# Performance work log

Hardware: AMD Instinct MI355X
Metric: run time of the kernel (lower is better)

The kernel has to match this reference:

```python
import jax, jax.numpy as jnp
import numpy as np

N_NODES = 1_000_000
N_EDGES = 20_000_000


def setup_inputs() -> dict:
    key = jax.random.key(0)
    k_row, k_col, k_attr = jax.random.split(key, 3)
    # Guarantee every row appears at least once so row-sums are > 0
    # (the original module implicitly assumes no zero-degree rows).
    row_tail = jax.random.randint(k_row, (N_EDGES - N_NODES,), 0, N_NODES, dtype=jnp.int32)
    row = jnp.concatenate([jnp.arange(N_NODES, dtype=jnp.int32), row_tail])
    col = jax.random.randint(k_col, (N_EDGES,), 0, N_NODES, dtype=jnp.int32)
    edge_index = jnp.stack([row, col])  # [2, E]
    # Positive edge weights keep the reciprocal well-conditioned.
    edge_attr = jax.random.uniform(k_attr, (N_EDGES,), dtype=jnp.float32,
                                   minval=0.1, maxval=1.0)
    return {"edge_index": edge_index, "edge_attr": edge_attr, "N": N_NODES}


def reference(edge_index, edge_attr, N):
    # spmm(edge_index, edge_attr, N, N, ones) == per-row sum of edge weights
    rowsum = jax.ops.segment_sum(edge_attr, edge_index[0], num_segments=N)  # [N]
    rownorm = 1.0 / rowsum                                                  # [N]
    # Gather normalization factor at the COLUMN index of each edge, then scale.
    return rownorm[edge_index[1]] * edge_attr                                # [E]
```

## Files before the change

kernel.cpp:

```cpp
#include <hip/hip_runtime.h>
#include <hip/hip_fp16.h>
#include <stdint.h>


typedef int      v4i __attribute__((ext_vector_type(4)));
typedef float    v4f __attribute__((ext_vector_type(4)));
typedef unsigned v4u __attribute__((ext_vector_type(4)));
using ull = unsigned long long;
using u16 = unsigned short;

#define BKT_BITS 13
#define BKT_W    (1 << BKT_BITS)
#define NB       128
#define NMAX     (NB << BKT_BITS)
#define TILE     4096
#define BLOCK1   512
#define BLOCK2   512


__global__ __launch_bounds__(BLOCK1) void hist_kernel(
    const int* __restrict__ row, int* __restrict__ histG, int E)
{
    __shared__ int h[NB];
    const int t = threadIdx.x;
    const long base = (long)blockIdx.x * TILE;
    if (t < NB) h[t] = 0;
    __syncthreads();
    if (base + TILE <= (long)E) {
        #pragma unroll
        for (int k = 0; k < 2; ++k) {
            const long e0 = base + ((long)(k * BLOCK1 + t) << 2);
            const v4i rv = *reinterpret_cast<const v4i*>(row + e0);
            atomicAdd(&h[rv.x >> BKT_BITS], 1);
            atomicAdd(&h[rv.y >> BKT_BITS], 1);
            atomicAdd(&h[rv.z >> BKT_BITS], 1);
            atomicAdd(&h[rv.w >> BKT_BITS], 1);
        }
    } else {
        for (int k = 0; k < 2; ++k) {
            const long e0 = base + ((long)(k * BLOCK1 + t) << 2);
            for (int j = 0; j < 4; ++j)
                if (e0 + j < (long)E) atomicAdd(&h[row[e0 + j] >> BKT_BITS], 1);
        }
    }
    __syncthreads();
    if (t < NB) histG[(size_t)blockIdx.x * NB + t] = h[t];
}

__global__ __launch_bounds__(256) void totals_kernel(
    const int* __restrict__ histG, int* __restrict__ totals, int nTiles)
{
    __shared__ int s[256];
    const int b = blockIdx.x;
    int acc = 0;
    for (int t = threadIdx.x; t < nTiles; t += 256)
        acc += histG[(size_t)t * NB + b];
    s[threadIdx.x] = acc;
    __syncthreads();
    for (int o = 128; o > 0; o >>= 1) {
        if (threadIdx.x < o) s[threadIdx.x] += s[threadIdx.x + o];
        __syncthreads();
    }
    if (threadIdx.x == 0) totals[b] = s[0];
}

__global__ __launch_bounds__(NB) void bases_kernel(
    const int* __restrict__ totals, int* __restrict__ bases)
{
    __shared__ int s[NB];
    const int t = threadIdx.x;
    const int rc = (totals[t] + 1) & ~1;
    s[t] = rc;
    __syncthreads();
    for (int off = 1; off < NB; off <<= 1) {
        const int v = (t >= off) ? s[t - off] : 0;
        __syncthreads();
        s[t] += v;
        __syncthreads();
    }
    bases[t] = s[t] - rc;
}

__global__ __launch_bounds__(256) void offsets_kernel(
    const int* __restrict__ histG, const int* __restrict__ bases,
    int* __restrict__ offG, int nTiles)
{
    __shared__ int s[256];
    const int b = blockIdx.x;
    const int seg = (nTiles + 255) >> 8;
    const int t0 = threadIdx.x * seg;
    int acc = 0;
    for (int k = 0; k < seg; ++k) {
        const int t = t0 + k;
        if (t < nTiles) acc += histG[(size_t)t * NB + b];
    }
    s[threadIdx.x] = acc;
    __syncthreads();
    for (int off = 1; off < 256; off <<= 1) {
        const int v = (threadIdx.x >= off) ? s[threadIdx.x - off] : 0;
        __syncthreads();
        s[threadIdx.x] += v;
        __syncthreads();
    }
    int run = bases[b] + s[threadIdx.x] - acc;
    for (int k = 0; k < seg; ++k) {
        const int t = t0 + k;
        if (t < nTiles) {
            offG[(size_t)t * NB + b] = run;
            run += histG[(size_t)t * NB + b];
        }
    }
}

__global__ __launch_bounds__(BLOCK1) void scatter_kernel(
    const int* __restrict__ row, const float* __restrict__ attr,
    const int* __restrict__ offG, ull* __restrict__ pairsG, int E)
{
    __shared__ int cnt[NB];
    __shared__ int scanb[NB];
    __shared__ int gbase[NB];
    __shared__ ull pairs[TILE];

    const int  t    = threadIdx.x;
    const long base = (long)blockIdx.x * TILE;
    const bool full = (base + TILE <= (long)E);

    if (t < NB) cnt[t] = 0;
    __syncthreads();

    int r[8]; float a[8]; int rk[8];
    if (full) {
        #pragma unroll
        for (int k = 0; k < 2; ++k) {
            const long e0 = base + ((long)(k * BLOCK1 + t) << 2);
            const v4i rv = *reinterpret_cast<const v4i*>(row + e0);
            const v4f av = __builtin_nontemporal_load(reinterpret_cast<const v4f*>(attr + e0));
            r[k*4+0]=rv.x; r[k*4+1]=rv.y; r[k*4+2]=rv.z; r[k*4+3]=rv.w;
            a[k*4+0]=av.x; a[k*4+1]=av.y; a[k*4+2]=av.z; a[k*4+3]=av.w;
        }
        #pragma unroll
        for (int i = 0; i < 8; ++i)
            rk[i] = atomicAdd(&cnt[r[i] >> BKT_BITS], 1);
    } else {
        for (int k = 0; k < 2; ++k) {
            const long e0 = base + ((long)(k * BLOCK1 + t) << 2);
            for (int j = 0; j < 4; ++j) {
                const int i = k*4 + j;
                if (e0 + j < (long)E) {
                    r[i] = row[e0 + j]; a[i] = attr[e0 + j];
                    rk[i] = atomicAdd(&cnt[r[i] >> BKT_BITS], 1);
                } else r[i] = -1;
            }
        }
    }
    __syncthreads();

    if (t < 64) {
        const int h0 = cnt[2*t], h1 = cnt[2*t+1];
        const int sum = h0 + h1;
        int x = sum;
        #pragma unroll
        for (int off = 1; off < 64; off <<= 1) {
            const int y = __shfl_up(x, off);
            if (t >= off) x += y;
        }
        const int excl = x - sum;
        scanb[2*t]   = excl;
        scanb[2*t+1] = excl + h0;
    }
    if (t < NB) gbase[t] = offG[(size_t)blockIdx.x * NB + t];
    __syncthreads();

    #pragma unroll
    for (int i = 0; i < 8; ++i)
        if (r[i] >= 0)
            pairs[scanb[r[i] >> BKT_BITS] + rk[i]] =
                ((ull)__float_as_uint(a[i]) << 32) | (unsigned)r[i];
    __syncthreads();

    const int total = full ? TILE : (int)((long)E - base);
    for (int s = t; s < total; s += BLOCK1) {
        const ull p  = pairs[s];
        const int bb = (int)(((unsigned)p) >> BKT_BITS);
        const size_t dst = (size_t)gbase[bb] + (size_t)(s - scanb[bb]);
        pairsG[dst] = p;
    }
}

__global__ __launch_bounds__(BLOCK2, 4) void reduce_kernel(
    const ull* __restrict__ pairsG, const int* __restrict__ totals,
    const int* __restrict__ bases, float* __restrict__ partial, int nSplit)
{
    __shared__ float bins[BKT_W];
    const int b = blockIdx.x / nSplit;
    const int q = blockIdx.x % nSplit;
    for (int i = threadIdx.x; i < BKT_W; i += BLOCK2) bins[i] = 0.0f;
    __syncthreads();

    const int cnt = totals[b];
    const ull* src = pairsG + (size_t)bases[b];

    const int Q16 = cnt >> 4;
    for (int i = q * BLOCK2 + threadIdx.x; i < Q16; i += nSplit * BLOCK2) {
        const v4u* p = reinterpret_cast<const v4u*>(src + ((size_t)i << 4));
        v4u v[8];
        #pragma unroll
        for (int k = 0; k < 8; ++k) v[k] = p[k];
        #pragma unroll
        for (int k = 0; k < 8; ++k) {
            atomicAdd(&bins[v[k].x & (BKT_W-1)], __uint_as_float(v[k].y));
            atomicAdd(&bins[v[k].z & (BKT_W-1)], __uint_as_float(v[k].w));
        }
    }
    const int tail0 = Q16 << 4;
    for (int o = tail0 + q * BLOCK2 + threadIdx.x; o < cnt; o += nSplit * BLOCK2) {
        const ull pp = src[o];
        atomicAdd(&bins[(unsigned)pp & (BKT_W-1)], __uint_as_float((unsigned)(pp >> 32)));
    }
    __syncthreads();

    float* dst = partial + (size_t)q * NMAX + ((size_t)b << BKT_BITS);
    for (int i = threadIdx.x; i < BKT_W; i += BLOCK2)
        dst[i] = bins[i];
}

__global__ void recip_kernel(const float* __restrict__ partial,
                             __half* __restrict__ rnorm16,
                             const int* __restrict__ Np, int nSplit) {
    const int N = *Np;
    const int stride = gridDim.x * blockDim.x;
    for (int i = blockIdx.x * blockDim.x + threadIdx.x; i < N; i += stride) {
        float s = 0.0f;
        for (int q = 0; q < nSplit; ++q) s += partial[(size_t)q * NMAX + i];
        rnorm16[i] = __float2half(1.0f / s);
    }
}


__global__ __launch_bounds__(256, 4) void gather_scale_f16_kernel(
    const int* __restrict__ col, const float* __restrict__ attr,
    const __half* __restrict__ rn, float* __restrict__ out, int E)
{
    const u16* rnu = reinterpret_cast<const u16*>(rn);
    const int tid = blockIdx.x * blockDim.x + threadIdx.x;
    const int stride = gridDim.x * blockDim.x;
    const int E4 = E >> 2;
    const v4i* col4  = reinterpret_cast<const v4i*>(col);
    const v4f* attr4 = reinterpret_cast<const v4f*>(attr);
    v4f*       out4  = reinterpret_cast<v4f*>(out);

    int i = tid;
    for (; i + 3 * stride < E4; i += 4 * stride) {
        v4i c[4]; v4f a[4];
        #pragma unroll
        for (int k = 0; k < 4; ++k) c[k] = __builtin_nontemporal_load(col4 + i + k * stride);
        #pragma unroll
        for (int k = 0; k < 4; ++k) a[k] = __builtin_nontemporal_load(attr4 + i + k * stride);
        u16 h[16];
        #pragma unroll
        for (int k = 0; k < 4; ++k) {
            h[k*4+0] = rnu[c[k].x];
            h[k*4+1] = rnu[c[k].y];
            h[k*4+2] = rnu[c[k].z];
            h[k*4+3] = rnu[c[k].w];
        }
        #pragma unroll
        for (int k = 0; k < 4; ++k) {
            v4f o;
            o.x = __half2float(__ushort_as_half(h[k*4+0])) * a[k].x;
            o.y = __half2float(__ushort_as_half(h[k*4+1])) * a[k].y;
            o.z = __half2float(__ushort_as_half(h[k*4+2])) * a[k].z;
            o.w = __half2float(__ushort_as_half(h[k*4+3])) * a[k].w;
            __builtin_nontemporal_store(o, out4 + i + k * stride);
        }
    }
    for (; i < E4; i += stride) {
        const v4i c = __builtin_nontemporal_load(col4 + i);
        const v4f a = __builtin_nontemporal_load(attr4 + i);
        v4f o;
        o.x = __half2float(rn[c.x]) * a.x; o.y = __half2float(rn[c.y]) * a.y;
        o.z = __half2float(rn[c.z]) * a.z; o.w = __half2float(rn[c.w]) * a.w;
        __builtin_nontemporal_store(o, out4 + i);
    }
    for (int e = (E4 << 2) + tid; e < E; e += stride)
        out[e] = __half2float(rn[col[e]]) * attr[e];
}


__global__ void zero_ws_kernel(float* __restrict__ ws, const int* __restrict__ Np) {
    const int N = *Np;
    const int stride = gridDim.x * blockDim.x;
    for (int i = blockIdx.x * blockDim.x + threadIdx.x; i < N; i += stride)
        ws[i] = 0.0f;
}

__global__ void rowsum_atomic_kernel(const int* __restrict__ row,
                                     const float* __restrict__ attr,
                                     float* __restrict__ rowsum, int E) {
    const int tid = blockIdx.x * blockDim.x + threadIdx.x;
    const int stride = gridDim.x * blockDim.x;
    const int E4 = E >> 2;
    for (int i = tid; i < E4; i += stride) {
        const int4   r = reinterpret_cast<const int4*>(row)[i];
        const float4 a = reinterpret_cast<const float4*>(attr)[i];
        atomicAdd(&rowsum[r.x], a.x);
        atomicAdd(&rowsum[r.y], a.y);
        atomicAdd(&rowsum[r.z], a.z);
        atomicAdd(&rowsum[r.w], a.w);
    }
    for (int i = (E4 << 2) + tid; i < E; i += stride)
        atomicAdd(&rowsum[row[i]], attr[i]);
}

__global__ void recip_fallback_kernel(float* __restrict__ rowsum,
                                      const int* __restrict__ Np) {
    const int N = *Np;
    const int stride = gridDim.x * blockDim.x;
    for (int i = blockIdx.x * blockDim.x + threadIdx.x; i < N; i += stride)
        rowsum[i] = 1.0f / rowsum[i];
}

__global__ __launch_bounds__(256) void gather_scale_f32_kernel(
    const int* __restrict__ col, const float* __restrict__ attr,
    const float* __restrict__ rnorm, float* __restrict__ out, int E)
{
    const int tid = blockIdx.x * blockDim.x + threadIdx.x;
    const int stride = gridDim.x * blockDim.x;
    const int E4 = E >> 2;
    const v4i* col4  = reinterpret_cast<const v4i*>(col);
    const v4f* attr4 = reinterpret_cast<const v4f*>(attr);
    v4f*       out4  = reinterpret_cast<v4f*>(out);
    for (int i = tid; i < E4; i += stride) {
        const v4i c = __builtin_nontemporal_load(col4 + i);
        const v4f a = __builtin_nontemporal_load(attr4 + i);
        v4f o;
        o.x = rnorm[c.x] * a.x; o.y = rnorm[c.y] * a.y;
        o.z = rnorm[c.z] * a.z; o.w = rnorm[c.w] * a.w;
        __builtin_nontemporal_store(o, out4 + i);
    }
    for (int e = (E4 << 2) + tid; e < E; e += stride)
        out[e] = rnorm[col[e]] * attr[e];
}


extern "C" void kernel_launch(void* const* d_in, const int* in_sizes, int n_in,
                              void* d_out, int out_size, void* d_ws, size_t ws_size,
                              hipStream_t stream) {
    const int*   edge_index = (const int*)d_in[0];
    const float* edge_attr  = (const float*)d_in[1];
    const int*   Np         = (const int*)d_in[2];

    const int E = in_sizes[1];
    const int* row = edge_index;
    const int* col = edge_index + E;
    float* out = (float*)d_out;

    const int nTiles = (E + TILE - 1) / TILE;
    auto align256 = [](size_t x) { return (x + 255) & ~(size_t)255; };

    size_t off = 0;
    const size_t basesOff  = off; off += align256(NB * sizeof(int));
    const size_t totalsOff = off; off += align256(NB * sizeof(int));
    const size_t rn16Off   = off; off += align256((size_t)NMAX * sizeof(__half));
    const size_t partOff   = off;
    const size_t histBytes = align256((size_t)nTiles * NB * sizeof(int));
    const size_t scanBytes = 2 * histBytes;
    const size_t pairsBytes = ((size_t)E + 2 * NB) * sizeof(ull);

    int nSplit = 0;
    size_t partRegion = 0;
    for (int c : {8, 4, 2, 1}) {
        size_t pr = (size_t)c * NMAX * sizeof(float);
        if (pr < scanBytes) pr = scanBytes;
        if (partOff + pr + pairsBytes <= ws_size) { nSplit = c; partRegion = pr; break; }
    }

    if (nSplit > 0) {
        int*    bases   = (int*)   ((char*)d_ws + basesOff);
        int*    totals  = (int*)   ((char*)d_ws + totalsOff);
        __half* rnorm16 = (__half*)((char*)d_ws + rn16Off);
        float*  partial = (float*) ((char*)d_ws + partOff);
        int*    histG   = (int*)   ((char*)d_ws + partOff);
        int*    offG    = (int*)   ((char*)d_ws + partOff + histBytes);
        ull*    pairs   = (ull*)   ((char*)d_ws + partOff + partRegion);

        hist_kernel           <<<nTiles, BLOCK1, 0, stream>>>(row, histG, E);
        totals_kernel         <<<NB, 256, 0, stream>>>(histG, totals, nTiles);
        bases_kernel          <<<1, NB, 0, stream>>>(totals, bases);
        offsets_kernel        <<<NB, 256, 0, stream>>>(histG, bases, offG, nTiles);
        scatter_kernel        <<<nTiles, BLOCK1, 0, stream>>>(row, edge_attr, offG, pairs, E);
        reduce_kernel         <<<NB * nSplit, BLOCK2, 0, stream>>>(pairs, totals, bases, partial, nSplit);
        recip_kernel          <<<1024, 256, 0, stream>>>(partial, rnorm16, Np, nSplit);
        gather_scale_f16_kernel<<<2048, 256, 0, stream>>>(col, edge_attr, rnorm16, out, E);
    } else {
        float* rowsum = (float*)d_ws;
        const int workE = (E + 3) >> 2;
        int gE = (workE + 255) / 256;
        if (gE > 2048) gE = 2048;
        zero_ws_kernel        <<<2048, 256, 0, stream>>>(rowsum, Np);
        rowsum_atomic_kernel  <<<gE, 256, 0, stream>>>(row, edge_attr, rowsum, E);
        recip_fallback_kernel <<<2048, 256, 0, stream>>>(rowsum, Np);
        gather_scale_f32_kernel<<<2048, 256, 0, stream>>>(col, edge_attr, rowsum, out, E);
    }
}
```

Before: 363.4 us.

## Use global_load_lds async staging in reduce and gather kernels, fp32 norms

The reduce kernel now streams bucketed (value,row) pairs into double-buffered LDS through global_load_lds. It waits on vmcnt so the next chunk's load overlaps the current chunk's shared atomics. The gather kernel issues its per-edge normalization lookups as direct-to-LDS 4-byte loads, one block per 2048-vec4 group, and the norms are stored as fp32 instead of fp16. The aim is better memory-level parallelism and less register pressure on the random gathers, at the cost of twice the norm table footprint and more LDS use, which may limit occupancy.

```diff
diff --git a/kernel.cpp b/kernel.cpp
--- a/kernel.cpp
+++ b/kernel.cpp
@@ -1,5 +1,4 @@
 #include <hip/hip_runtime.h>
-#include <hip/hip_fp16.h>
 #include <stdint.h>
 
 
@@ -7,7 +6,6 @@
 typedef float    v4f __attribute__((ext_vector_type(4)));
 typedef unsigned v4u __attribute__((ext_vector_type(4)));
 using ull = unsigned long long;
-using u16 = unsigned short;
 
 #define BKT_BITS 13
 #define BKT_W    (1 << BKT_BITS)
@@ -16,6 +14,8 @@
 #define TILE     4096
 #define BLOCK1   512
 #define BLOCK2   512
+
+#define GLD_LDS(G, L, SZ) __builtin_amdgcn_global_load_lds((G), (L), (SZ), 0, 0)
 
 
 __global__ __launch_bounds__(BLOCK1) void hist_kernel(
@@ -187,103 +187,126 @@
     }
 }
 
-__global__ __launch_bounds__(BLOCK2, 4) void reduce_kernel(
+__global__ __launch_bounds__(BLOCK2) void reduce_kernel(
     const ull* __restrict__ pairsG, const int* __restrict__ totals,
     const int* __restrict__ bases, float* __restrict__ partial, int nSplit)
 {
     __shared__ float bins[BKT_W];
+    __shared__ ull   stage[2][2048];
     const int b = blockIdx.x / nSplit;
     const int q = blockIdx.x % nSplit;
-    for (int i = threadIdx.x; i < BKT_W; i += BLOCK2) bins[i] = 0.0f;
+    const int t = threadIdx.x;
+    const int w = t >> 6, l = t & 63;
+
+    for (int i = t; i < BKT_W; i += BLOCK2) bins[i] = 0.0f;
     __syncthreads();
 
     const int cnt = totals[b];
     const ull* src = pairsG + (size_t)bases[b];
-
-    const int Q16 = cnt >> 4;
-    for (int i = q * BLOCK2 + threadIdx.x; i < Q16; i += nSplit * BLOCK2) {
-        const v4u* p = reinterpret_cast<const v4u*>(src + ((size_t)i << 4));
-        v4u v[8];
-        #pragma unroll
-        for (int k = 0; k < 8; ++k) v[k] = p[k];
-        #pragma unroll
-        for (int k = 0; k < 8; ++k) {
-            atomicAdd(&bins[v[k].x & (BKT_W-1)], __uint_as_float(v[k].y));
-            atomicAdd(&bins[v[k].z & (BKT_W-1)], __uint_as_float(v[k].w));
-        }
-    }
-    const int tail0 = Q16 << 4;
-    for (int o = tail0 + q * BLOCK2 + threadIdx.x; o < cnt; o += nSplit * BLOCK2) {
-        const ull pp = src[o];
-        atomicAdd(&bins[(unsigned)pp & (BKT_W-1)], __uint_as_float((unsigned)(pp >> 32)));
+    const int nChunks = cnt >> 11;
+
+    int k = q;
+    int cur = 0;
+    if (k < nChunks) {
+        const ull* gp = src + ((size_t)k << 11) + (w << 8);
+        GLD_LDS(gp + l*2,       &stage[cur][(w << 8)],       16);
+        GLD_LDS(gp + 128 + l*2, &stage[cur][(w << 8) + 128], 16);
+    }
+    while (k < nChunks) {
+        const int kn = k + nSplit;
+        if (kn < nChunks) {
+            const ull* gp = src + ((size_t)kn << 11) + (w << 8);
+            GLD_LDS(gp + l*2,       &stage[cur ^ 1][(w << 8)],       16);
+            GLD_LDS(gp + 128 + l*2, &stage[cur ^ 1][(w << 8) + 128], 16);
+            asm volatile("s_waitcnt vmcnt(2)" ::: "memory");
+        } else {
+            asm volatile("s_waitcnt vmcnt(0)" ::: "memory");
+        }
+        __builtin_amdgcn_sched_barrier(0);
+        const v4u* sp = reinterpret_cast<const v4u*>(&stage[cur][(w << 8) + l*4]);
+        const v4u x0 = sp[0];
+        const v4u x1 = sp[1];
+        atomicAdd(&bins[x0.x & (BKT_W-1)], __uint_as_float(x0.y));
+        atomicAdd(&bins[x0.z & (BKT_W-1)], __uint_as_float(x0.w));
+        atomicAdd(&bins[x1.x & (BKT_W-1)], __uint_as_float(x1.y));
+        atomicAdd(&bins[x1.z & (BKT_W-1)], __uint_as_float(x1.w));
+        cur ^= 1;
+        k = kn;
+    }
+
+    if (q == 0) {
+        for (int o = (nChunks << 11) + t; o < cnt; o += BLOCK2) {
+            const ull p = src[o];
+            atomicAdd(&bins[(unsigned)p & (BKT_W-1)], __uint_as_float((unsigned)(p >> 32)));
+        }
     }
     __syncthreads();
 
     float* dst = partial + (size_t)q * NMAX + ((size_t)b << BKT_BITS);
-    for (int i = threadIdx.x; i < BKT_W; i += BLOCK2)
+    for (int i = t; i < BKT_W; i += BLOCK2)
         dst[i] = bins[i];
 }
 
 __global__ void recip_kernel(const float* __restrict__ partial,
-                             __half* __restrict__ rnorm16,
+                             float* __restrict__ rnF,
                              const int* __restrict__ Np, int nSplit) {
     const int N = *Np;
     const int stride = gridDim.x * blockDim.x;
     for (int i = blockIdx.x * blockDim.x + threadIdx.x; i < N; i += stride) {
         float s = 0.0f;
         for (int q = 0; q < nSplit; ++q) s += partial[(size_t)q * NMAX + i];
-        rnorm16[i] = __float2half(1.0f / s);
-    }
-}
-
-
-__global__ __launch_bounds__(256, 4) void gather_scale_f16_kernel(
+        rnF[i] = 1.0f / s;
+    }
+}
+
+__global__ __launch_bounds__(256, 4) void gather_gld_kernel(
     const int* __restrict__ col, const float* __restrict__ attr,
-    const __half* __restrict__ rn, float* __restrict__ out, int E)
-{
-    const u16* rnu = reinterpret_cast<const u16*>(rn);
-    const int tid = blockIdx.x * blockDim.x + threadIdx.x;
-    const int stride = gridDim.x * blockDim.x;
+    const float* __restrict__ rnF, float* __restrict__ out, int E)
+{
+    __shared__ float gstage[4][32][64];
+    const int t = threadIdx.x, w = t >> 6, l = t & 63;
     const int E4 = E >> 2;
     const v4i* col4  = reinterpret_cast<const v4i*>(col);
     const v4f* attr4 = reinterpret_cast<const v4f*>(attr);
     v4f*       out4  = reinterpret_cast<v4f*>(out);
-
-    int i = tid;
-    for (; i + 3 * stride < E4; i += 4 * stride) {
-        v4i c[4]; v4f a[4];
-        #pragma unroll
-        for (int k = 0; k < 4; ++k) c[k] = __builtin_nontemporal_load(col4 + i + k * stride);
-        #pragma unroll
-        for (int k = 0; k < 4; ++k) a[k] = __builtin_nontemporal_load(attr4 + i + k * stride);
-        u16 h[16];
-        #pragma unroll
-        for (int k = 0; k < 4; ++k) {
-            h[k*4+0] = rnu[c[k].x];
-            h[k*4+1] = rnu[c[k].y];
-            h[k*4+2] = rnu[c[k].z];
-            h[k*4+3] = rnu[c[k].w];
-        }
-        #pragma unroll
-        for (int k = 0; k < 4; ++k) {
-            v4f o;
-            o.x = __half2float(__ushort_as_half(h[k*4+0])) * a[k].x;
-            o.y = __half2float(__ushort_as_half(h[k*4+1])) * a[k].y;
-            o.z = __half2float(__ushort_as_half(h[k*4+2])) * a[k].z;
-            o.w = __half2float(__ushort_as_half(h[k*4+3])) * a[k].w;
-            __builtin_nontemporal_store(o, out4 + i + k * stride);
-        }
-    }
-    for (; i < E4; i += stride) {
-        const v4i c = __builtin_nontemporal_load(col4 + i);
-        const v4f a = __builtin_nontemporal_load(attr4 + i);
-        v4f o;
-        o.x = __half2float(rn[c.x]) * a.x; o.y = __half2float(rn[c.y]) * a.y;
-        o.z = __half2float(rn[c.z]) * a.z; o.w = __half2float(rn[c.w]) * a.w;
-        __builtin_nontemporal_store(o, out4 + i);
-    }
-    for (int e = (E4 << 2) + tid; e < E; e += stride)
-        out[e] = __half2float(rn[col[e]]) * attr[e];
+    const int groups = (E4 + 2047) >> 11;
+
+    for (int g = blockIdx.x; g < groups; g += gridDim.x) {
+        const int q0 = (g << 11) + t;
+        v4i c[8]; v4f a[8];
+        #pragma unroll
+        for (int j = 0; j < 8; ++j) {
+            const int qi = q0 + (j << 8);
+            const int s = qi < E4 ? qi : 0;
+            c[j] = __builtin_nontemporal_load(col4 + s);
+            a[j] = __builtin_nontemporal_load(attr4 + s);
+        }
+        #pragma unroll
+        for (int j = 0; j < 8; ++j) {
+            GLD_LDS(rnF + c[j].x, &gstage[w][j*4+0][0], 4);
+            GLD_LDS(rnF + c[j].y, &gstage[w][j*4+1][0], 4);
+            GLD_LDS(rnF + c[j].z, &gstage[w][j*4+2][0], 4);
+            GLD_LDS(rnF + c[j].w, &gstage[w][j*4+3][0], 4);
+        }
+        asm volatile("s_waitcnt vmcnt(0)" ::: "memory");
+        __builtin_amdgcn_sched_barrier(0);
+        #pragma unroll
+        for (int j = 0; j < 8; ++j) {
+            const int qi = q0 + (j << 8);
+            if (qi < E4) {
+                v4f o;
+                o.x = gstage[w][j*4+0][l] * a[j].x;
+                o.y = gstage[w][j*4+1][l] * a[j].y;
+                o.z = gstage[w][j*4+2][l] * a[j].z;
+                o.w = gstage[w][j*4+3][l] * a[j].w;
+                __builtin_nontemporal_store(o, out4 + qi);
+            }
+        }
+    }
+    if (blockIdx.x == 0 && t < (E & 3)) {
+        const int e = (E4 << 2) + t;
+        out[e] = rnF[col[e]] * attr[e];
+    }
 }
 
 
@@ -361,7 +384,7 @@
     size_t off = 0;
     const size_t basesOff  = off; off += align256(NB * sizeof(int));
     const size_t totalsOff = off; off += align256(NB * sizeof(int));
-    const size_t rn16Off   = off; off += align256((size_t)NMAX * sizeof(__half));
+    const size_t rnOff     = off; off += align256((size_t)NMAX * sizeof(float));
     const size_t partOff   = off;
     const size_t histBytes = align256((size_t)nTiles * NB * sizeof(int));
     const size_t scanBytes = 2 * histBytes;
@@ -376,22 +399,24 @@
     }
 
     if (nSplit > 0) {
-        int*    bases   = (int*)   ((char*)d_ws + basesOff);
-        int*    totals  = (int*)   ((char*)d_ws + totalsOff);
-        __half* rnorm16 = (__half*)((char*)d_ws + rn16Off);
-        float*  partial = (float*) ((char*)d_ws + partOff);
-        int*    histG   = (int*)   ((char*)d_ws + partOff);
-        int*    offG    = (int*)   ((char*)d_ws + partOff + histBytes);
-        ull*    pairs   = (ull*)   ((char*)d_ws + partOff + partRegion);
-
-        hist_kernel           <<<nTiles, BLOCK1, 0, stream>>>(row, histG, E);
-        totals_kernel         <<<NB, 256, 0, stream>>>(histG, totals, nTiles);
-        bases_kernel          <<<1, NB, 0, stream>>>(totals, bases);
-        offsets_kernel        <<<NB, 256, 0, stream>>>(histG, bases, offG, nTiles);
-        scatter_kernel        <<<nTiles, BLOCK1, 0, stream>>>(row, edge_attr, offG, pairs, E);
-        reduce_kernel         <<<NB * nSplit, BLOCK2, 0, stream>>>(pairs, totals, bases, partial, nSplit);
-        recip_kernel          <<<1024, 256, 0, stream>>>(partial, rnorm16, Np, nSplit);
-        gather_scale_f16_kernel<<<2048, 256, 0, stream>>>(col, edge_attr, rnorm16, out, E);
+        int*   bases   = (int*)  ((char*)d_ws + basesOff);
+        int*   totals  = (int*)  ((char*)d_ws + totalsOff);
+        float* rnF     = (float*)((char*)d_ws + rnOff);
+        float* partial = (float*)((char*)d_ws + partOff);
+        int*   histG   = (int*)  ((char*)d_ws + partOff);
+        int*   offG    = (int*)  ((char*)d_ws + partOff + histBytes);
+        ull*   pairs   = (ull*)  ((char*)d_ws + partOff + partRegion);
+
+        const int gGroups = ((E >> 2) + 2047) >> 11;
+
+        hist_kernel      <<<nTiles, BLOCK1, 0, stream>>>(row, histG, E);
+        totals_kernel    <<<NB, 256, 0, stream>>>(histG, totals, nTiles);
+        bases_kernel     <<<1, NB, 0, stream>>>(totals, bases);
+        offsets_kernel   <<<NB, 256, 0, stream>>>(histG, bases, offG, nTiles);
+        scatter_kernel   <<<nTiles, BLOCK1, 0, stream>>>(row, edge_attr, offG, pairs, E);
+        reduce_kernel    <<<NB * nSplit, BLOCK2, 0, stream>>>(pairs, totals, bases, partial, nSplit);
+        recip_kernel     <<<1024, 256, 0, stream>>>(partial, rnF, Np, nSplit);
+        gather_gld_kernel<<<gGroups, 256, 0, stream>>>(col, edge_attr, rnF, out, E);
     } else {
         float* rowsum = (float*)d_ws;
         const int workE = (E + 3) >> 2;
```

New measurement: 379.3 us. 4.4% more time.
